# Kernel optimization log

Measured on AMD Instinct MI355X. Metric: run time of the kernel, lower is better.

The kernel has to match this reference:

```python
import jax, jax.numpy as jnp
import numpy as np

WINDOW_SIZE = 11
CHANNEL = 3
SIGMA = 1.5
C1 = 0.01 ** 2
C2 = 0.03 ** 2


def _make_window():
    coords = jnp.arange(WINDOW_SIZE, dtype=jnp.float32) - WINDOW_SIZE // 2
    g = jnp.exp(-coords ** 2 / (2 * SIGMA ** 2))
    g = g / g.sum()
    w2d = jnp.outer(g, g)                      # (K, K)
    # (C, 1, K, K) depthwise kernel, OIHW with feature_group_count=C
    return jnp.broadcast_to(w2d[None, None], (CHANNEL, 1, WINDOW_SIZE, WINDOW_SIZE))


def _dwconv(x, w):
    # x: (1, C, H, W), w: (C, 1, K, K) -> same-padded depthwise conv
    pad = WINDOW_SIZE // 2
    return jax.lax.conv_general_dilated(
        x, w, window_strides=(1, 1), padding=[(pad, pad), (pad, pad)],
        feature_group_count=CHANNEL,
        dimension_numbers=('NCHW', 'OIHW', 'NCHW'))


def setup_inputs() -> dict:
    key = jax.random.key(0)
    k1, k2 = jax.random.split(key)
    H = W = 2048
    img1 = jax.random.uniform(k1, (H, W, 3), dtype=jnp.float32)
    img2 = jax.random.uniform(k2, (H, W, 3), dtype=jnp.float32)
    window = _make_window()
    return {"img1": img1, "img2": img2, "window": window}


def reference(img1, img2, window):
    # (H, W, C) -> (1, C, H, W)
    x = jnp.transpose(img1, (2, 0, 1))[None]
    y = jnp.transpose(img2, (2, 0, 1))[None]

    mu1 = _dwconv(x, window)
    mu2 = _dwconv(y, window)
    mu1_sq = mu1 ** 2
    mu2_sq = mu2 ** 2
    mu12 = mu1 * mu2

    sigma1_sq = _dwconv(x * x, window) - mu1_sq
    sigma2_sq = _dwconv(y * y, window) - mu2_sq
    sigma12 = _dwconv(x * y, window) - mu12

    ssim_map = ((2 * mu12 + C1) * (2 * sigma12 + C2)) / (
        (mu1_sq + mu2_sq + C1) * (sigma1_sq + sigma2_sq + C2))
    return 1.0 - ssim_map.mean()
```

## Files before the change

### kernel.cpp

```cpp
#include <hip/hip_runtime.h>
#include <math.h>

#define TILE 32
#define HALO 5
#define IH   42
#define LDSW 44
#define HBW  36

__global__ void zero_kernel(float* ws) { ws[0] = 0.0f; }

__global__ void finalize_kernel(const float* ws, float* out, float inv_n) {
    out[0] = 1.0f - ws[0] * inv_n;
}

__global__ __launch_bounds__(256, 3) void ssim_kernel(
    const float* __restrict__ img1, const float* __restrict__ img2,
    const float* __restrict__ window, float* __restrict__ accum,
    int H, int W)
{
    __shared__ float sx[IH][LDSW];
    __shared__ float sy[IH][LDSW];
    __shared__ float hb[5][IH][HBW];
    __shared__ float wsum[4];

    const int tid = threadIdx.x;
    const int x0  = blockIdx.x * TILE;
    const int y0  = blockIdx.y * TILE;

    float gr[11];
    {
        float inv = 1.0f / sqrtf(window[60]);
        #pragma unroll
        for (int t = 0; t < 11; ++t) gr[t] = window[55 + t] * inv;
    }

    float acc = 0.0f;

    for (int c = 0; c < 3; ++c) {
        __syncthreads();

        for (int item = tid; item < IH * 11; item += 256) {
            int r   = item / 11;
            int j4  = (item % 11) * 4;
            int gh  = y0 + r - HALO;
            int gx0 = x0 + j4 - HALO;
            bool rowok = ((unsigned)gh < (unsigned)H);
            float vx[4], vy[4];
            #pragma unroll
            for (int k = 0; k < 4; ++k) {
                int gx = gx0 + k;
                bool ok = rowok && ((unsigned)gx < (unsigned)W);
                long off = ((long)gh * W + gx) * 3 + c;
                vx[k] = ok ? img1[off] : 0.0f;
                vy[k] = ok ? img2[off] : 0.0f;
            }
            *(float4*)&sx[r][j4] = make_float4(vx[0], vx[1], vx[2], vx[3]);
            *(float4*)&sy[r][j4] = make_float4(vy[0], vy[1], vy[2], vy[3]);
        }
        __syncthreads();

        for (int item = tid; item < IH * 8; item += 256) {
            int r  = item >> 3;
            int j4 = (item & 7) * 4;
            float xv[16], yv[16];
            *(float4*)&xv[0]  = *(const float4*)&sx[r][j4];
            *(float4*)&xv[4]  = *(const float4*)&sx[r][j4 + 4];
            *(float4*)&xv[8]  = *(const float4*)&sx[r][j4 + 8];
            *(float4*)&xv[12] = *(const float4*)&sx[r][j4 + 12];
            *(float4*)&yv[0]  = *(const float4*)&sy[r][j4];
            *(float4*)&yv[4]  = *(const float4*)&sy[r][j4 + 4];
            *(float4*)&yv[8]  = *(const float4*)&sy[r][j4 + 8];
            *(float4*)&yv[12] = *(const float4*)&sy[r][j4 + 12];

            float xx[14], yy[14], xy[14];
            #pragma unroll
            for (int t = 0; t < 14; ++t) {
                xx[t] = xv[t] * xv[t];
                yy[t] = yv[t] * yv[t];
                xy[t] = xv[t] * yv[t];
            }
            float h0[4] = {0,0,0,0}, h1[4] = {0,0,0,0}, h2[4] = {0,0,0,0};
            float h3[4] = {0,0,0,0}, h4[4] = {0,0,0,0};
            #pragma unroll
            for (int jj = 0; jj < 4; ++jj) {
                #pragma unroll
                for (int t = 0; t < 11; ++t) {
                    float g = gr[t];
                    h0[jj] += g * xv[jj + t];
                    h1[jj] += g * yv[jj + t];
                    h2[jj] += g * xx[jj + t];
                    h3[jj] += g * yy[jj + t];
                    h4[jj] += g * xy[jj + t];
                }
            }
            *(float4*)&hb[0][r][j4] = make_float4(h0[0], h0[1], h0[2], h0[3]);
            *(float4*)&hb[1][r][j4] = make_float4(h1[0], h1[1], h1[2], h1[3]);
            *(float4*)&hb[2][r][j4] = make_float4(h2[0], h2[1], h2[2], h2[3]);
            *(float4*)&hb[3][r][j4] = make_float4(h3[0], h3[1], h3[2], h3[3]);
            *(float4*)&hb[4][r][j4] = make_float4(h4[0], h4[1], h4[2], h4[3]);
        }
        __syncthreads();

        {
            int j  = tid & 31;
            int i0 = (tid >> 5) * 4;
            float m1[4]  = {0,0,0,0}, m2[4]  = {0,0,0,0};
            float v11[4] = {0,0,0,0}, v22[4] = {0,0,0,0}, v12[4] = {0,0,0,0};
            #pragma unroll
            for (int t = 0; t < 14; ++t) {
                float b0 = hb[0][i0 + t][j];
                float b1 = hb[1][i0 + t][j];
                float b2 = hb[2][i0 + t][j];
                float b3 = hb[3][i0 + t][j];
                float b4 = hb[4][i0 + t][j];
                #pragma unroll
                for (int o = 0; o < 4; ++o) {
                    if (t - o >= 0 && t - o <= 10) {
                        float g = gr[t - o];
                        m1[o]  += g * b0;
                        m2[o]  += g * b1;
                        v11[o] += g * b2;
                        v22[o] += g * b3;
                        v12[o] += g * b4;
                    }
                }
            }
            const float C1 = 0.0001f, C2 = 0.0009f;
            #pragma unroll
            for (int o = 0; o < 4; ++o) {
                int gy = y0 + i0 + o, gx = x0 + j;
                if (gy < H && gx < W) {
                    float mu1 = m1[o], mu2 = m2[o];
                    float mu11 = mu1 * mu1, mu22 = mu2 * mu2, mu12 = mu1 * mu2;
                    float s11 = v11[o] - mu11;
                    float s22 = v22[o] - mu22;
                    float s12 = v12[o] - mu12;
                    float num = (2.0f * mu12 + C1) * (2.0f * s12 + C2);
                    float den = (mu11 + mu22 + C1) * (s11 + s22 + C2);
                    acc += num / den;
                }
            }
        }
    }

    #pragma unroll
    for (int off = 32; off > 0; off >>= 1)
        acc += __shfl_down(acc, off, 64);
    int lane = tid & 63, wid = tid >> 6;
    if (lane == 0) wsum[wid] = acc;
    __syncthreads();
    if (tid == 0)
        atomicAdd(accum, wsum[0] + wsum[1] + wsum[2] + wsum[3]);
}

extern "C" void kernel_launch(void* const* d_in, const int* in_sizes, int n_in,
                              void* d_out, int out_size, void* d_ws, size_t ws_size,
                              hipStream_t stream) {
    const float* img1   = (const float*)d_in[0];
    const float* img2   = (const float*)d_in[1];
    const float* window = (const float*)d_in[2];
    float* out = (float*)d_out;
    float* ws  = (float*)d_ws;

    long hw = (long)in_sizes[0] / 3;
    int W = (int)(sqrt((double)hw) + 0.5);
    int H = (int)(hw / W);

    float inv_n = (float)(1.0 / ((double)H * (double)W * 3.0));

    dim3 grid((W + TILE - 1) / TILE, (H + TILE - 1) / TILE);

    zero_kernel<<<1, 1, 0, stream>>>(ws);
    ssim_kernel<<<grid, 256, 0, stream>>>(img1, img2, window, ws, H, W);
    finalize_kernel<<<1, 1, 0, stream>>>(ws, out, inv_n);
}
```

Measured before the change: 216.1 us.

## Shrink tile height, add interior fast path, replace atomics with partial-sum reduction

Tile height drops from 32 to 16 rows, which cuts LDS use so launch bounds can ask for more resident blocks, at the price of a larger halo overhead per output. Interior blocks skip the per-element bounds checks when loading. The single global atomic is replaced by per-block partial sums in the workspace and a one-block reduction kernel, which also removes the zero kernel. The vertical pass now uses only half the threads, which lowers arithmetic parallelism per block.

```diff
diff --git a/kernel.cpp b/kernel.cpp
--- a/kernel.cpp
+++ b/kernel.cpp
@@ -1,9 +1,10 @@
 #include <hip/hip_runtime.h>
 #include <math.h>
 
-#define TILE 32
+#define TILE_W 32
+#define TILE_H 16
 #define HALO 5
-#define IH   42
+#define IH   26
 #define LDSW 44
 #define HBW  36
 
@@ -13,10 +14,27 @@
     out[0] = 1.0f - ws[0] * inv_n;
 }
 
-__global__ __launch_bounds__(256, 3) void ssim_kernel(
+__global__ void reduce_kernel(const float* __restrict__ ws, float* __restrict__ out,
+                              int n, float inv_n) {
+    __shared__ float s[16];
+    float a = 0.0f;
+    for (int i = threadIdx.x; i < n; i += 1024) a += ws[i];
+    #pragma unroll
+    for (int off = 32; off > 0; off >>= 1) a += __shfl_down(a, off, 64);
+    if ((threadIdx.x & 63) == 0) s[threadIdx.x >> 6] = a;
+    __syncthreads();
+    if (threadIdx.x == 0) {
+        float t = 0.0f;
+        #pragma unroll
+        for (int w = 0; w < 16; ++w) t += s[w];
+        out[0] = 1.0f - t * inv_n;
+    }
+}
+
+__global__ __launch_bounds__(256, 5) void ssim_kernel(
     const float* __restrict__ img1, const float* __restrict__ img2,
-    const float* __restrict__ window, float* __restrict__ accum,
-    int H, int W)
+    const float* __restrict__ window, float* __restrict__ ws,
+    int H, int W, int use_partials)
 {
     __shared__ float sx[IH][LDSW];
     __shared__ float sy[IH][LDSW];
@@ -24,8 +42,8 @@
     __shared__ float wsum[4];
 
     const int tid = threadIdx.x;
-    const int x0  = blockIdx.x * TILE;
-    const int y0  = blockIdx.y * TILE;
+    const int x0  = blockIdx.x * TILE_W;
+    const int y0  = blockIdx.y * TILE_H;
 
     float gr[11];
     {
@@ -34,34 +52,53 @@
         for (int t = 0; t < 11; ++t) gr[t] = window[55 + t] * inv;
     }
 
+    const bool interior = (x0 >= HALO) && (x0 + 39 <= W) &&
+                          (y0 >= HALO) && (y0 + 21 <= H);
+
     float acc = 0.0f;
 
     for (int c = 0; c < 3; ++c) {
         __syncthreads();
 
-        for (int item = tid; item < IH * 11; item += 256) {
-            int r   = item / 11;
-            int j4  = (item % 11) * 4;
-            int gh  = y0 + r - HALO;
-            int gx0 = x0 + j4 - HALO;
-            bool rowok = ((unsigned)gh < (unsigned)H);
-            float vx[4], vy[4];
-            #pragma unroll
-            for (int k = 0; k < 4; ++k) {
-                int gx = gx0 + k;
-                bool ok = rowok && ((unsigned)gx < (unsigned)W);
-                long off = ((long)gh * W + gx) * 3 + c;
-                vx[k] = ok ? img1[off] : 0.0f;
-                vy[k] = ok ? img2[off] : 0.0f;
-            }
-            *(float4*)&sx[r][j4] = make_float4(vx[0], vx[1], vx[2], vx[3]);
-            *(float4*)&sy[r][j4] = make_float4(vy[0], vy[1], vy[2], vy[3]);
+        if (interior) {
+            for (int item = tid; item < IH * 11; item += 256) {
+                int r   = item / 11;
+                int j4  = (item % 11) * 4;
+                long base = ((long)(y0 + r - HALO) * W + (x0 + j4 - HALO)) * 3 + c;
+                float vx[4], vy[4];
+                #pragma unroll
+                for (int k = 0; k < 4; ++k) {
+                    vx[k] = img1[base + 3 * k];
+                    vy[k] = img2[base + 3 * k];
+                }
+                *(float4*)&sx[r][j4] = make_float4(vx[0], vx[1], vx[2], vx[3]);
+                *(float4*)&sy[r][j4] = make_float4(vy[0], vy[1], vy[2], vy[3]);
+            }
+        } else {
+            for (int item = tid; item < IH * 11; item += 256) {
+                int r   = item / 11;
+                int j4  = (item % 11) * 4;
+                int gh  = y0 + r - HALO;
+                int gx0 = x0 + j4 - HALO;
+                bool rowok = ((unsigned)gh < (unsigned)H);
+                float vx[4], vy[4];
+                #pragma unroll
+                for (int k = 0; k < 4; ++k) {
+                    int gx = gx0 + k;
+                    bool ok = rowok && ((unsigned)gx < (unsigned)W);
+                    long off = ((long)gh * W + gx) * 3 + c;
+                    vx[k] = ok ? img1[off] : 0.0f;
+                    vy[k] = ok ? img2[off] : 0.0f;
+                }
+                *(float4*)&sx[r][j4] = make_float4(vx[0], vx[1], vx[2], vx[3]);
+                *(float4*)&sy[r][j4] = make_float4(vy[0], vy[1], vy[2], vy[3]);
+            }
         }
         __syncthreads();
 
-        for (int item = tid; item < IH * 8; item += 256) {
-            int r  = item >> 3;
-            int j4 = (item & 7) * 4;
+        if (tid < IH * 8) {
+            int r  = tid >> 3;
+            int j4 = (tid & 7) * 4;
             float xv[16], yv[16];
             *(float4*)&xv[0]  = *(const float4*)&sx[r][j4];
             *(float4*)&xv[4]  = *(const float4*)&sx[r][j4 + 4];
@@ -101,7 +138,7 @@
         }
         __syncthreads();
 
-        {
+        if (tid < 128) {
             int j  = tid & 31;
             int i0 = (tid >> 5) * 4;
             float m1[4]  = {0,0,0,0}, m2[4]  = {0,0,0,0};
@@ -149,8 +186,13 @@
     int lane = tid & 63, wid = tid >> 6;
     if (lane == 0) wsum[wid] = acc;
     __syncthreads();
-    if (tid == 0)
-        atomicAdd(accum, wsum[0] + wsum[1] + wsum[2] + wsum[3]);
+    if (tid == 0) {
+        float total = wsum[0] + wsum[1] + wsum[2] + wsum[3];
+        if (use_partials)
+            ws[blockIdx.y * gridDim.x + blockIdx.x] = total;
+        else
+            atomicAdd(ws, total);
+    }
 }
 
 extern "C" void kernel_launch(void* const* d_in, const int* in_sizes, int n_in,
@@ -168,9 +210,16 @@
 
     float inv_n = (float)(1.0 / ((double)H * (double)W * 3.0));
 
-    dim3 grid((W + TILE - 1) / TILE, (H + TILE - 1) / TILE);
-
-    zero_kernel<<<1, 1, 0, stream>>>(ws);
-    ssim_kernel<<<grid, 256, 0, stream>>>(img1, img2, window, ws, H, W);
-    finalize_kernel<<<1, 1, 0, stream>>>(ws, out, inv_n);
-}
+    dim3 grid((W + TILE_W - 1) / TILE_W, (H + TILE_H - 1) / TILE_H);
+    int nblocks = grid.x * grid.y;
+    int use_partials = (ws_size >= (size_t)nblocks * sizeof(float)) ? 1 : 0;
+
+    if (use_partials) {
+        ssim_kernel<<<grid, 256, 0, stream>>>(img1, img2, window, ws, H, W, 1);
+        reduce_kernel<<<1, 1024, 0, stream>>>(ws, out, nblocks, inv_n);
+    } else {
+        zero_kernel<<<1, 1, 0, stream>>>(ws);
+        ssim_kernel<<<grid, 256, 0, stream>>>(img1, img2, window, ws, H, W, 0);
+        finalize_kernel<<<1, 1, 0, stream>>>(ws, out, inv_n);
+    }
+}
```

Result: slower. 359.0 us (+66.1%).
